# Kernel tuning notes

Measured on AMD Instinct MI355X. Metric: run time of the kernel, lower is better.

The kernel has to match this reference:

```python
import jax, jax.numpy as jnp
import numpy as np


def setup_inputs() -> dict:
    key = jax.random.key(0)
    k1, k2, k3 = jax.random.split(key, 3)
    B, N, D = 16, 2048, 128
    q = jax.random.normal(k1, (B, N, D), dtype=jnp.float32)
    k = jax.random.normal(k2, (B, D, N), dtype=jnp.float32)
    v = jax.random.normal(k3, (B, N, D), dtype=jnp.float32)
    return {"q": q, "k": k, "v": v}


def reference(q, k, v):
    # scores: [B, N, N] — note NO 1/sqrt(d) scaling, matching the source
    scores = jnp.einsum('bnd,bdm->bnm', q, k)
    probs = jax.nn.softmax(scores, axis=-1)
    out = jnp.einsum('bnm,bmd->bnd', probs, v)  # [B, N, D]
    return out
```

## Files before the change

### kernel.cpp

```cpp
#include <hip/hip_runtime.h>
#include <hip/hip_bf16.h>


typedef __attribute__((ext_vector_type(8))) _Float16 f16x8;
typedef __attribute__((ext_vector_type(4))) float f32x4;

constexpr int Bz = 16;
constexpr int Nn = 2048;
constexpr int Dd = 128;
constexpr int BM = 128;
constexpr int BN = 64;
constexpr int PK = 72;

__device__ __forceinline__ int swz(int r) { return (r ^ (r >> 3)) & 7; }

__device__ __forceinline__ uint packh2(float a, float b) {
    union { _Float16 h[2]; uint u; } p;
    p.h[0] = (_Float16)a; p.h[1] = (_Float16)b;
    return p.u;
}

__global__ __launch_bounds__(512, 2)
void fattn_kernel(const float* __restrict__ qg,
                  const float* __restrict__ kg,
                  const float* __restrict__ vg,
                  float* __restrict__ og)
{
    __shared__ ushort lds_k[BN * Dd];
    __shared__ ushort lds_v[Dd * BN];
    __shared__ ushort lds_p[8 * 16 * PK];
    uint* const lds_k32 = (uint*)lds_k;
    uint* const lds_v32 = (uint*)lds_v;

    const int bid  = blockIdx.x;
    const int xcd  = bid & 7;
    const int idx  = bid >> 3;
    const int b    = xcd * 2 + (idx >> 4);
    const int q0   = (idx & 15) * BM;
    const int tid  = threadIdx.x;
    const int wv   = tid >> 6;
    const int lane = tid & 63;
    const int quad = lane >> 4;
    const int l15  = lane & 15;

    f16x8 qf[4];
    {
        const float* qp = qg + (size_t)(b * Nn + q0 + wv * 16 + l15) * Dd + quad * 8;
        #pragma unroll
        for (int c = 0; c < 4; ++c) {
            float4 x0 = *(const float4*)(qp + c * 32);
            float4 x1 = *(const float4*)(qp + c * 32 + 4);
            const float xv[8] = {x0.x, x0.y, x0.z, x0.w, x1.x, x1.y, x1.z, x1.w};
            union { f16x8 v; _Float16 e[8]; } u;
            #pragma unroll
            for (int j = 0; j < 8; ++j) u.e[j] = (_Float16)xv[j];
            qf[c] = u.v;
        }
    }

    f32x4 accO[8];
    #pragma unroll
    for (int i = 0; i < 8; ++i) accO[i] = f32x4{0.f, 0.f, 0.f, 0.f};
    float m_i = -1e30f, l_i = 0.f;

    const int kgrp = tid & 7;
    const int krow = tid >> 3;
    const int vgrp = tid & 15;
    const int vrow = tid >> 4;

    const float* kbase = kg + (size_t)b * Dd * Nn;
    const float* vbase = vg + (size_t)b * Nn * Dd;

    float4 kr[4], vr[4];
    auto issue_loads = [&](int n0) {
        const int d0 = krow * 2;
        const float* s0 = kbase + (size_t)d0 * Nn + n0 + kgrp * 8;
        kr[0] = ((const float4*)s0)[0];
        kr[1] = ((const float4*)s0)[1];
        kr[2] = ((const float4*)(s0 + Nn))[0];
        kr[3] = ((const float4*)(s0 + Nn))[1];
        const int kk0 = vrow * 2;
        const float* t0 = vbase + (size_t)(n0 + kk0) * Dd + vgrp * 8;
        vr[0] = ((const float4*)t0)[0];
        vr[1] = ((const float4*)t0)[1];
        vr[2] = ((const float4*)(t0 + Dd))[0];
        vr[3] = ((const float4*)(t0 + Dd))[1];
    };
    auto write_lds = [&]() {
        const int d0 = krow * 2;
        const float* av = (const float*)&kr[0];
        const float* bv = (const float*)&kr[2];
        #pragma unroll
        for (int j = 0; j < 8; ++j) {
            const int n = kgrp * 8 + j;
            lds_k32[n * (Dd / 2) + ((d0 >> 1) ^ (swz(n) << 2))] = packh2(av[j], bv[j]);
        }
        const int kk0 = vrow * 2;
        const float* cv = (const float*)&vr[0];
        const float* dv = (const float*)&vr[2];
        #pragma unroll
        for (int j = 0; j < 8; ++j) {
            const int dd = vgrp * 8 + j;
            lds_v32[dd * (BN / 2) + ((kk0 >> 1) ^ (swz(dd) << 2))] = packh2(cv[j], dv[j]);
        }
    };

    issue_loads(0);

    for (int it = 0; it < Nn / BN; ++it) {
        write_lds();
        __syncthreads();

        issue_loads(((it + 1) & 31) * BN);

        f32x4 accS[4];
        #pragma unroll
        for (int kt = 0; kt < 4; ++kt) {
            f32x4 s = f32x4{0.f, 0.f, 0.f, 0.f};
            const int row = kt * 16 + l15;
            const int sw = swz(row) << 3;
            #pragma unroll
            for (int c = 0; c < 4; ++c) {
                f16x8 kf = *(const f16x8*)&lds_k[row * Dd + ((c * 32 + quad * 8) ^ sw)];
                s = __builtin_amdgcn_mfma_f32_16x16x32_f16(kf, qf[c], s, 0, 0, 0);
            }
            accS[kt] = s;
        }

        float mx = accS[0][0];
        #pragma unroll
        for (int kt = 0; kt < 4; ++kt)
            #pragma unroll
            for (int r = 0; r < 4; ++r)
                mx = fmaxf(mx, accS[kt][r]);
        mx = fmaxf(mx, __shfl_xor(mx, 16, 64));
        mx = fmaxf(mx, __shfl_xor(mx, 32, 64));
        const float mn = fmaxf(m_i, mx);
        const float alpha = __expf(m_i - mn);
        m_i = mn;
        float local = 0.f;
        #pragma unroll
        for (int kt = 0; kt < 4; ++kt)
            #pragma unroll
            for (int r = 0; r < 4; ++r) {
                const float p = __expf(accS[kt][r] - mn);
                accS[kt][r] = p;
                local += p;
            }
        l_i = l_i * alpha + local;
        #pragma unroll
        for (int dt = 0; dt < 8; ++dt)
            #pragma unroll
            for (int r = 0; r < 4; ++r)
                accO[dt][r] *= alpha;

        ushort* pl = lds_p + wv * 16 * PK;
        #pragma unroll
        for (int kt = 0; kt < 4; ++kt) {
            uint2 w;
            w.x = packh2(accS[kt][0], accS[kt][1]);
            w.y = packh2(accS[kt][2], accS[kt][3]);
            *(uint2*)(pl + l15 * PK + kt * 16 + quad * 4) = w;
        }
        f16x8 pf0 = *(const f16x8*)&pl[l15 * PK + quad * 8];
        f16x8 pf1 = *(const f16x8*)&pl[l15 * PK + 32 + quad * 8];

        #pragma unroll
        for (int dt = 0; dt < 8; ++dt) {
            const int row = dt * 16 + l15;
            const int sw = swz(row) << 3;
            f16x8 vf0 = *(const f16x8*)&lds_v[row * BN + ((quad * 8) ^ sw)];
            f16x8 vf1 = *(const f16x8*)&lds_v[row * BN + ((32 + quad * 8) ^ sw)];
            accO[dt] = __builtin_amdgcn_mfma_f32_16x16x32_f16(vf0, pf0, accO[dt], 0, 0, 0);
            accO[dt] = __builtin_amdgcn_mfma_f32_16x16x32_f16(vf1, pf1, accO[dt], 0, 0, 0);
        }
        __syncthreads();
    }

    float l = l_i;
    l += __shfl_xor(l, 16, 64);
    l += __shfl_xor(l, 32, 64);
    const float inv = 1.f / l;
    float* ob = og + (size_t)(b * Nn + q0 + wv * 16 + l15) * Dd;
    #pragma unroll
    for (int dt = 0; dt < 8; ++dt) {
        float4 val;
        val.x = accO[dt][0] * inv;
        val.y = accO[dt][1] * inv;
        val.z = accO[dt][2] * inv;
        val.w = accO[dt][3] * inv;
        *(float4*)(ob + dt * 16 + quad * 4) = val;
    }
}

extern "C" void kernel_launch(void* const* d_in, const int* in_sizes, int n_in,
                              void* d_out, int out_size, void* d_ws, size_t ws_size,
                              hipStream_t stream) {
    const float* q = (const float*)d_in[0];
    const float* k = (const float*)d_in[1];
    const float* v = (const float*)d_in[2];
    float* o = (float*)d_out;
    (void)d_ws; (void)ws_size; (void)in_sizes; (void)n_in; (void)out_size;
    fattn_kernel<<<dim3(Bz * (Nn / BM)), dim3(512), 0, stream>>>(q, k, v, o);
}
```

Before: 150.9 us.

## Warp-specialize producer/consumer waves with double-buffered LDS and 32x32 MFMA

Splits the 8 waves into 4 producer waves that load K/V from global memory, convert them to fp16 and write a double-buffered LDS tile, and 4 consumer waves that each handle 32 query rows using 32x32x16 MFMA. The KV tile shrinks to 32 keys per iteration, with a new swizzle for the V layout. The aim is to overlap global loads with compute and to use larger MFMA tiles. In exchange, half the waves do no math, there are twice as many iterations and barriers, and consumers hold more accumulator registers.

```diff
diff --git a/kernel.cpp b/kernel.cpp
--- a/kernel.cpp
+++ b/kernel.cpp
@@ -3,16 +3,17 @@
 
 
 typedef __attribute__((ext_vector_type(8))) _Float16 f16x8;
-typedef __attribute__((ext_vector_type(4))) float f32x4;
+typedef __attribute__((ext_vector_type(16))) float f32x16;
 
 constexpr int Bz = 16;
 constexpr int Nn = 2048;
 constexpr int Dd = 128;
 constexpr int BM = 128;
-constexpr int BN = 64;
-constexpr int PK = 72;
+constexpr int BN = 32;
+constexpr int PK = 40;
 
 __device__ __forceinline__ int swz(int r) { return (r ^ (r >> 3)) & 7; }
+__device__ __forceinline__ int sw4(int d) { return ((d >> 1) ^ (d >> 3)) & 3; }
 
 __device__ __forceinline__ uint packh2(float a, float b) {
     union { _Float16 h[2]; uint u; } p;
@@ -26,11 +27,9 @@
                   const float* __restrict__ vg,
                   float* __restrict__ og)
 {
-    __shared__ ushort lds_k[BN * Dd];
-    __shared__ ushort lds_v[Dd * BN];
-    __shared__ ushort lds_p[8 * 16 * PK];
-    uint* const lds_k32 = (uint*)lds_k;
-    uint* const lds_v32 = (uint*)lds_v;
+    __shared__ ushort lds_k[2][BN * Dd];
+    __shared__ ushort lds_v[2][Dd * BN];
+    __shared__ ushort lds_p[4][32 * PK];
 
     const int bid  = blockIdx.x;
     const int xcd  = bid & 7;
@@ -40,38 +39,19 @@
     const int tid  = threadIdx.x;
     const int wv   = tid >> 6;
     const int lane = tid & 63;
-    const int quad = lane >> 4;
-    const int l15  = lane & 15;
-
-    f16x8 qf[4];
-    {
-        const float* qp = qg + (size_t)(b * Nn + q0 + wv * 16 + l15) * Dd + quad * 8;
-        #pragma unroll
-        for (int c = 0; c < 4; ++c) {
-            float4 x0 = *(const float4*)(qp + c * 32);
-            float4 x1 = *(const float4*)(qp + c * 32 + 4);
-            const float xv[8] = {x0.x, x0.y, x0.z, x0.w, x1.x, x1.y, x1.z, x1.w};
-            union { f16x8 v; _Float16 e[8]; } u;
-            #pragma unroll
-            for (int j = 0; j < 8; ++j) u.e[j] = (_Float16)xv[j];
-            qf[c] = u.v;
-        }
-    }
-
-    f32x4 accO[8];
-    #pragma unroll
-    for (int i = 0; i < 8; ++i) accO[i] = f32x4{0.f, 0.f, 0.f, 0.f};
-    float m_i = -1e30f, l_i = 0.f;
-
-    const int kgrp = tid & 7;
-    const int krow = tid >> 3;
-    const int vgrp = tid & 15;
-    const int vrow = tid >> 4;
-
+    const int h    = lane >> 5;
+    const int l31  = lane & 31;
+    const bool producer = (wv >= 4);
+
+    const int ptid = (wv - 4) * 64 + lane;
+    const int kgrp = ptid & 3;
+    const int krow = ptid >> 2;
+    const int vgrp = ptid & 15;
+    const int vrow = ptid >> 4;
     const float* kbase = kg + (size_t)b * Dd * Nn;
     const float* vbase = vg + (size_t)b * Nn * Dd;
-
     float4 kr[4], vr[4];
+
     auto issue_loads = [&](int n0) {
         const int d0 = krow * 2;
         const float* s0 = kbase + (size_t)d0 * Nn + n0 + kgrp * 8;
@@ -86,110 +66,137 @@
         vr[2] = ((const float4*)(t0 + Dd))[0];
         vr[3] = ((const float4*)(t0 + Dd))[1];
     };
-    auto write_lds = [&]() {
-        const int d0 = krow * 2;
+    auto write_lds = [&](int buf) {
+        uint* kw = (uint*)lds_k[buf];
         const float* av = (const float*)&kr[0];
         const float* bv = (const float*)&kr[2];
         #pragma unroll
         for (int j = 0; j < 8; ++j) {
             const int n = kgrp * 8 + j;
-            lds_k32[n * (Dd / 2) + ((d0 >> 1) ^ (swz(n) << 2))] = packh2(av[j], bv[j]);
-        }
-        const int kk0 = vrow * 2;
+            kw[n * (Dd / 2) + (krow ^ (swz(n) << 2))] = packh2(av[j], bv[j]);
+        }
+        uint* vw = (uint*)lds_v[buf];
         const float* cv = (const float*)&vr[0];
         const float* dv = (const float*)&vr[2];
         #pragma unroll
         for (int j = 0; j < 8; ++j) {
             const int dd = vgrp * 8 + j;
-            lds_v32[dd * (BN / 2) + ((kk0 >> 1) ^ (swz(dd) << 2))] = packh2(cv[j], dv[j]);
+            vw[dd * (BN / 2) + (vrow ^ (sw4(dd) << 2))] = packh2(cv[j], dv[j]);
         }
     };
 
-    issue_loads(0);
-
-    for (int it = 0; it < Nn / BN; ++it) {
-        write_lds();
+    f16x8 qf[8];
+    if (!producer) {
+        const float* qp = qg + (size_t)(b * Nn + q0 + wv * 32 + l31) * Dd + h * 8;
+        #pragma unroll
+        for (int c = 0; c < 8; ++c) {
+            float4 x0 = *(const float4*)(qp + c * 16);
+            float4 x1 = *(const float4*)(qp + c * 16 + 4);
+            const float xv[8] = {x0.x, x0.y, x0.z, x0.w, x1.x, x1.y, x1.z, x1.w};
+            union { f16x8 v; _Float16 e[8]; } u;
+            #pragma unroll
+            for (int j = 0; j < 8; ++j) u.e[j] = (_Float16)xv[j];
+            qf[c] = u.v;
+        }
+    }
+    f32x16 accO[4];
+    #pragma unroll
+    for (int dt = 0; dt < 4; ++dt)
+        #pragma unroll
+        for (int r = 0; r < 16; ++r) accO[dt][r] = 0.f;
+    float m_i = -1e30f, l_i = 0.f;
+
+    if (producer) {
+        issue_loads(0);
+        write_lds(0);
+    }
+    __syncthreads();
+
+    constexpr int ITERS = Nn / BN;
+    for (int it = 0; it < ITERS; ++it) {
+        const int cur = it & 1;
+        if (producer) {
+            if (it + 1 < ITERS) {
+                issue_loads((it + 1) * BN);
+                write_lds(cur ^ 1);
+            }
+        } else {
+            const ushort* kb = lds_k[cur];
+            const ushort* vb = lds_v[cur];
+
+            f32x16 accS;
+            #pragma unroll
+            for (int r = 0; r < 16; ++r) accS[r] = 0.f;
+            {
+                const int kkrow = l31;
+                const int sw = swz(kkrow) << 3;
+                #pragma unroll
+                for (int c = 0; c < 8; ++c) {
+                    f16x8 kf = *(const f16x8*)&kb[kkrow * Dd + ((c * 16 + h * 8) ^ sw)];
+                    accS = __builtin_amdgcn_mfma_f32_32x32x16_f16(kf, qf[c], accS, 0, 0, 0);
+                }
+            }
+
+            float mx = accS[0];
+            #pragma unroll
+            for (int r = 1; r < 16; ++r) mx = fmaxf(mx, accS[r]);
+            mx = fmaxf(mx, __shfl_xor(mx, 32, 64));
+            const float mn = fmaxf(m_i, mx);
+            const float alpha = __expf(m_i - mn);
+            m_i = mn;
+            float local = 0.f;
+            #pragma unroll
+            for (int r = 0; r < 16; ++r) {
+                const float p = __expf(accS[r] - mn);
+                accS[r] = p;
+                local += p;
+            }
+            l_i = l_i * alpha + local;
+            #pragma unroll
+            for (int dt = 0; dt < 4; ++dt)
+                #pragma unroll
+                for (int r = 0; r < 16; ++r) accO[dt][r] *= alpha;
+
+            ushort* pl = lds_p[wv];
+            #pragma unroll
+            for (int g = 0; g < 4; ++g) {
+                uint2 w;
+                w.x = packh2(accS[4 * g + 0], accS[4 * g + 1]);
+                w.y = packh2(accS[4 * g + 2], accS[4 * g + 3]);
+                *(uint2*)(pl + l31 * PK + 8 * g + 4 * h) = w;
+            }
+            f16x8 pf0 = *(const f16x8*)&pl[l31 * PK + 8 * h];
+            f16x8 pf1 = *(const f16x8*)&pl[l31 * PK + 16 + 8 * h];
+
+            #pragma unroll
+            for (int dt = 0; dt < 4; ++dt) {
+                const int drow = dt * 32 + l31;
+                const int sv = sw4(drow) << 3;
+                f16x8 vf0 = *(const f16x8*)&vb[drow * BN + ((8 * h) ^ sv)];
+                f16x8 vf1 = *(const f16x8*)&vb[drow * BN + ((16 + 8 * h) ^ sv)];
+                accO[dt] = __builtin_amdgcn_mfma_f32_32x32x16_f16(vf0, pf0, accO[dt], 0, 0, 0);
+                accO[dt] = __builtin_amdgcn_mfma_f32_32x32x16_f16(vf1, pf1, accO[dt], 0, 0, 0);
+            }
+        }
         __syncthreads();
-
-        issue_loads(((it + 1) & 31) * BN);
-
-        f32x4 accS[4];
-        #pragma unroll
-        for (int kt = 0; kt < 4; ++kt) {
-            f32x4 s = f32x4{0.f, 0.f, 0.f, 0.f};
-            const int row = kt * 16 + l15;
-            const int sw = swz(row) << 3;
-            #pragma unroll
-            for (int c = 0; c < 4; ++c) {
-                f16x8 kf = *(const f16x8*)&lds_k[row * Dd + ((c * 32 + quad * 8) ^ sw)];
-                s = __builtin_amdgcn_mfma_f32_16x16x32_f16(kf, qf[c], s, 0, 0, 0);
-            }
-            accS[kt] = s;
-        }
-
-        float mx = accS[0][0];
-        #pragma unroll
-        for (int kt = 0; kt < 4; ++kt)
-            #pragma unroll
-            for (int r = 0; r < 4; ++r)
-                mx = fmaxf(mx, accS[kt][r]);
-        mx = fmaxf(mx, __shfl_xor(mx, 16, 64));
-        mx = fmaxf(mx, __shfl_xor(mx, 32, 64));
-        const float mn = fmaxf(m_i, mx);
-        const float alpha = __expf(m_i - mn);
-        m_i = mn;
-        float local = 0.f;
-        #pragma unroll
-        for (int kt = 0; kt < 4; ++kt)
-            #pragma unroll
-            for (int r = 0; r < 4; ++r) {
-                const float p = __expf(accS[kt][r] - mn);
-                accS[kt][r] = p;
-                local += p;
-            }
-        l_i = l_i * alpha + local;
-        #pragma unroll
-        for (int dt = 0; dt < 8; ++dt)
-            #pragma unroll
-            for (int r = 0; r < 4; ++r)
-                accO[dt][r] *= alpha;
-
-        ushort* pl = lds_p + wv * 16 * PK;
-        #pragma unroll
-        for (int kt = 0; kt < 4; ++kt) {
-            uint2 w;
-            w.x = packh2(accS[kt][0], accS[kt][1]);
-            w.y = packh2(accS[kt][2], accS[kt][3]);
-            *(uint2*)(pl + l15 * PK + kt * 16 + quad * 4) = w;
-        }
-        f16x8 pf0 = *(const f16x8*)&pl[l15 * PK + quad * 8];
-        f16x8 pf1 = *(const f16x8*)&pl[l15 * PK + 32 + quad * 8];
-
-        #pragma unroll
-        for (int dt = 0; dt < 8; ++dt) {
-            const int row = dt * 16 + l15;
-            const int sw = swz(row) << 3;
-            f16x8 vf0 = *(const f16x8*)&lds_v[row * BN + ((quad * 8) ^ sw)];
-            f16x8 vf1 = *(const f16x8*)&lds_v[row * BN + ((32 + quad * 8) ^ sw)];
-            accO[dt] = __builtin_amdgcn_mfma_f32_16x16x32_f16(vf0, pf0, accO[dt], 0, 0, 0);
-            accO[dt] = __builtin_amdgcn_mfma_f32_16x16x32_f16(vf1, pf1, accO[dt], 0, 0, 0);
-        }
-        __syncthreads();
-    }
-
-    float l = l_i;
-    l += __shfl_xor(l, 16, 64);
-    l += __shfl_xor(l, 32, 64);
-    const float inv = 1.f / l;
-    float* ob = og + (size_t)(b * Nn + q0 + wv * 16 + l15) * Dd;
-    #pragma unroll
-    for (int dt = 0; dt < 8; ++dt) {
-        float4 val;
-        val.x = accO[dt][0] * inv;
-        val.y = accO[dt][1] * inv;
-        val.z = accO[dt][2] * inv;
-        val.w = accO[dt][3] * inv;
-        *(float4*)(ob + dt * 16 + quad * 4) = val;
+    }
+
+    if (!producer) {
+        float l = l_i + __shfl_xor(l_i, 32, 64);
+        const float inv = 1.f / l;
+        float* ob = og + (size_t)(b * Nn + q0 + wv * 32 + l31) * Dd;
+        #pragma unroll
+        for (int dt = 0; dt < 4; ++dt) {
+            #pragma unroll
+            for (int g = 0; g < 4; ++g) {
+                float4 val;
+                val.x = accO[dt][4 * g + 0] * inv;
+                val.y = accO[dt][4 * g + 1] * inv;
+                val.z = accO[dt][4 * g + 2] * inv;
+                val.w = accO[dt][4 * g + 3] * inv;
+                *(float4*)(ob + dt * 32 + 8 * g + 4 * h) = val;
+            }
+        }
     }
 }
 
```

Result: faster. 145.0 us (-3.9%).

## Split KV range across two wave groups per block with LDS merge

Applied to the files above, without the earlier changes.

Halves the query tile to 64 rows and KV tile to 32, and splits each block's 8 waves into two groups that each process half of the key/value sequence, merging the partial softmax states through shared memory at the end. This doubles the grid size and raises the occupancy hint to 4 blocks per CU, aiming for more parallelism and latency hiding. The register prefetch of the next tile is dropped, so global loads are no longer overlapped with compute. Each block also reuses every K/V tile across fewer query rows, which adds global traffic and an extra merge step.

```diff
diff --git a/kernel.cpp b/kernel.cpp
--- a/kernel.cpp
+++ b/kernel.cpp
@@ -8,11 +8,14 @@
 constexpr int Bz = 16;
 constexpr int Nn = 2048;
 constexpr int Dd = 128;
-constexpr int BM = 128;
-constexpr int BN = 64;
-constexpr int PK = 72;
+constexpr int BM = 64;
+constexpr int BN = 32;
+constexpr int HALF = Nn / 2;
+constexpr int ITERS = HALF / BN;
+constexpr int PK = 40;
 
 __device__ __forceinline__ int swz(int r) { return (r ^ (r >> 3)) & 7; }
+__device__ __forceinline__ int sw4(int d) { return ((d >> 1) ^ (d >> 3)) & 3; }
 
 __device__ __forceinline__ uint packh2(float a, float b) {
     union { _Float16 h[2]; uint u; } p;
@@ -20,32 +23,44 @@
     return p.u;
 }
 
-__global__ __launch_bounds__(512, 2)
+__global__ __launch_bounds__(512, 4)
 void fattn_kernel(const float* __restrict__ qg,
                   const float* __restrict__ kg,
                   const float* __restrict__ vg,
                   float* __restrict__ og)
 {
-    __shared__ ushort lds_k[BN * Dd];
-    __shared__ ushort lds_v[Dd * BN];
-    __shared__ ushort lds_p[8 * 16 * PK];
-    uint* const lds_k32 = (uint*)lds_k;
-    uint* const lds_v32 = (uint*)lds_v;
+    __shared__ ushort smem[21504];
 
     const int bid  = blockIdx.x;
     const int xcd  = bid & 7;
     const int idx  = bid >> 3;
-    const int b    = xcd * 2 + (idx >> 4);
-    const int q0   = (idx & 15) * BM;
+    const int b    = xcd * 2 + (idx >> 5);
+    const int q0   = (idx & 31) * BM;
     const int tid  = threadIdx.x;
     const int wv   = tid >> 6;
     const int lane = tid & 63;
     const int quad = lane >> 4;
     const int l15  = lane & 15;
+    const int w    = wv & 3;
+    const int g    = wv >> 2;
+
+    ushort* const kb = smem + g * 4096;
+    ushort* const vb = smem + 8192 + g * 4096;
+    ushort* const pl = smem + 16384 + wv * 640;
+    uint* const kw = (uint*)kb;
+    uint* const vw = (uint*)vb;
+
+    const int gtid = tid & 255;
+    const int kgN = (gtid & 3) * 8;
+    const int kdp = gtid >> 2;
+    const int vgD = (gtid & 15) * 8;
+    const int vkp = gtid >> 4;
+    const float* kbase = kg + (size_t)b * Dd * Nn;
+    const float* vbase = vg + (size_t)b * Nn * Dd;
 
     f16x8 qf[4];
     {
-        const float* qp = qg + (size_t)(b * Nn + q0 + wv * 16 + l15) * Dd + quad * 8;
+        const float* qp = qg + (size_t)(b * Nn + q0 + w * 16 + l15) * Dd + quad * 8;
         #pragma unroll
         for (int c = 0; c < 4; ++c) {
             float4 x0 = *(const float4*)(qp + c * 32);
@@ -57,82 +72,53 @@
             qf[c] = u.v;
         }
     }
-
     f32x4 accO[8];
     #pragma unroll
     for (int i = 0; i < 8; ++i) accO[i] = f32x4{0.f, 0.f, 0.f, 0.f};
     float m_i = -1e30f, l_i = 0.f;
 
-    const int kgrp = tid & 7;
-    const int krow = tid >> 3;
-    const int vgrp = tid & 15;
-    const int vrow = tid >> 4;
-
-    const float* kbase = kg + (size_t)b * Dd * Nn;
-    const float* vbase = vg + (size_t)b * Nn * Dd;
-
-    float4 kr[4], vr[4];
-    auto issue_loads = [&](int n0) {
-        const int d0 = krow * 2;
-        const float* s0 = kbase + (size_t)d0 * Nn + n0 + kgrp * 8;
-        kr[0] = ((const float4*)s0)[0];
-        kr[1] = ((const float4*)s0)[1];
-        kr[2] = ((const float4*)(s0 + Nn))[0];
-        kr[3] = ((const float4*)(s0 + Nn))[1];
-        const int kk0 = vrow * 2;
-        const float* t0 = vbase + (size_t)(n0 + kk0) * Dd + vgrp * 8;
-        vr[0] = ((const float4*)t0)[0];
-        vr[1] = ((const float4*)t0)[1];
-        vr[2] = ((const float4*)(t0 + Dd))[0];
-        vr[3] = ((const float4*)(t0 + Dd))[1];
-    };
-    auto write_lds = [&]() {
-        const int d0 = krow * 2;
-        const float* av = (const float*)&kr[0];
-        const float* bv = (const float*)&kr[2];
-        #pragma unroll
-        for (int j = 0; j < 8; ++j) {
-            const int n = kgrp * 8 + j;
-            lds_k32[n * (Dd / 2) + ((d0 >> 1) ^ (swz(n) << 2))] = packh2(av[j], bv[j]);
-        }
-        const int kk0 = vrow * 2;
-        const float* cv = (const float*)&vr[0];
-        const float* dv = (const float*)&vr[2];
-        #pragma unroll
-        for (int j = 0; j < 8; ++j) {
-            const int dd = vgrp * 8 + j;
-            lds_v32[dd * (BN / 2) + ((kk0 >> 1) ^ (swz(dd) << 2))] = packh2(cv[j], dv[j]);
-        }
-    };
-
-    issue_loads(0);
-
-    for (int it = 0; it < Nn / BN; ++it) {
-        write_lds();
+    for (int it = 0; it < ITERS; ++it) {
+        const int n0 = g * HALF + it * BN;
+        {
+            const float* s0 = kbase + (size_t)(2 * kdp) * Nn + n0 + kgN;
+            float4 a0 = ((const float4*)s0)[0], a1 = ((const float4*)s0)[1];
+            float4 b0 = ((const float4*)(s0 + Nn))[0], b1 = ((const float4*)(s0 + Nn))[1];
+            const float av[8] = {a0.x, a0.y, a0.z, a0.w, a1.x, a1.y, a1.z, a1.w};
+            const float bv[8] = {b0.x, b0.y, b0.z, b0.w, b1.x, b1.y, b1.z, b1.w};
+            #pragma unroll
+            for (int j = 0; j < 8; ++j) {
+                const int n = kgN + j;
+                kw[n * 64 + (kdp ^ (swz(n) << 2))] = packh2(av[j], bv[j]);
+            }
+            const float* t0 = vbase + (size_t)(n0 + 2 * vkp) * Dd + vgD;
+            float4 c0 = ((const float4*)t0)[0], c1 = ((const float4*)t0)[1];
+            float4 d0 = ((const float4*)(t0 + Dd))[0], d1 = ((const float4*)(t0 + Dd))[1];
+            const float cv[8] = {c0.x, c0.y, c0.z, c0.w, c1.x, c1.y, c1.z, c1.w};
+            const float dv[8] = {d0.x, d0.y, d0.z, d0.w, d1.x, d1.y, d1.z, d1.w};
+            #pragma unroll
+            for (int j = 0; j < 8; ++j) {
+                const int dd = vgD + j;
+                vw[dd * 16 + (vkp ^ (sw4(dd) << 2))] = packh2(cv[j], dv[j]);
+            }
+        }
         __syncthreads();
 
-        issue_loads(((it + 1) & 31) * BN);
-
-        f32x4 accS[4];
-        #pragma unroll
-        for (int kt = 0; kt < 4; ++kt) {
+        f32x4 accS[2];
+        #pragma unroll
+        for (int kt = 0; kt < 2; ++kt) {
             f32x4 s = f32x4{0.f, 0.f, 0.f, 0.f};
             const int row = kt * 16 + l15;
             const int sw = swz(row) << 3;
             #pragma unroll
             for (int c = 0; c < 4; ++c) {
-                f16x8 kf = *(const f16x8*)&lds_k[row * Dd + ((c * 32 + quad * 8) ^ sw)];
+                f16x8 kf = *(const f16x8*)&kb[row * 128 + ((c * 32 + quad * 8) ^ sw)];
                 s = __builtin_amdgcn_mfma_f32_16x16x32_f16(kf, qf[c], s, 0, 0, 0);
             }
             accS[kt] = s;
         }
 
-        float mx = accS[0][0];
-        #pragma unroll
-        for (int kt = 0; kt < 4; ++kt)
-            #pragma unroll
-            for (int r = 0; r < 4; ++r)
-                mx = fmaxf(mx, accS[kt][r]);
+        float mx = fmaxf(fmaxf(fmaxf(accS[0][0], accS[0][1]), fmaxf(accS[0][2], accS[0][3])),
+                         fmaxf(fmaxf(accS[1][0], accS[1][1]), fmaxf(accS[1][2], accS[1][3])));
         mx = fmaxf(mx, __shfl_xor(mx, 16, 64));
         mx = fmaxf(mx, __shfl_xor(mx, 32, 64));
         const float mn = fmaxf(m_i, mx);
@@ -140,7 +126,7 @@
         m_i = mn;
         float local = 0.f;
         #pragma unroll
-        for (int kt = 0; kt < 4; ++kt)
+        for (int kt = 0; kt < 2; ++kt)
             #pragma unroll
             for (int r = 0; r < 4; ++r) {
                 const float p = __expf(accS[kt][r] - mn);
@@ -151,45 +137,67 @@
         #pragma unroll
         for (int dt = 0; dt < 8; ++dt)
             #pragma unroll
-            for (int r = 0; r < 4; ++r)
-                accO[dt][r] *= alpha;
-
-        ushort* pl = lds_p + wv * 16 * PK;
-        #pragma unroll
-        for (int kt = 0; kt < 4; ++kt) {
-            uint2 w;
-            w.x = packh2(accS[kt][0], accS[kt][1]);
-            w.y = packh2(accS[kt][2], accS[kt][3]);
-            *(uint2*)(pl + l15 * PK + kt * 16 + quad * 4) = w;
-        }
-        f16x8 pf0 = *(const f16x8*)&pl[l15 * PK + quad * 8];
-        f16x8 pf1 = *(const f16x8*)&pl[l15 * PK + 32 + quad * 8];
+            for (int r = 0; r < 4; ++r) accO[dt][r] *= alpha;
+
+        #pragma unroll
+        for (int kt = 0; kt < 2; ++kt) {
+            uint2 pw;
+            pw.x = packh2(accS[kt][0], accS[kt][1]);
+            pw.y = packh2(accS[kt][2], accS[kt][3]);
+            *(uint2*)(pl + l15 * PK + kt * 16 + quad * 4) = pw;
+        }
+        f16x8 pf = *(const f16x8*)&pl[l15 * PK + quad * 8];
 
         #pragma unroll
         for (int dt = 0; dt < 8; ++dt) {
-            const int row = dt * 16 + l15;
-            const int sw = swz(row) << 3;
-            f16x8 vf0 = *(const f16x8*)&lds_v[row * BN + ((quad * 8) ^ sw)];
-            f16x8 vf1 = *(const f16x8*)&lds_v[row * BN + ((32 + quad * 8) ^ sw)];
-            accO[dt] = __builtin_amdgcn_mfma_f32_16x16x32_f16(vf0, pf0, accO[dt], 0, 0, 0);
-            accO[dt] = __builtin_amdgcn_mfma_f32_16x16x32_f16(vf1, pf1, accO[dt], 0, 0, 0);
+            const int drow = dt * 16 + l15;
+            const int sv = sw4(drow) << 3;
+            f16x8 vf = *(const f16x8*)&vb[drow * 32 + ((quad * 8) ^ sv)];
+            accO[dt] = __builtin_amdgcn_mfma_f32_16x16x32_f16(vf, pf, accO[dt], 0, 0, 0);
         }
         __syncthreads();
     }
 
-    float l = l_i;
-    l += __shfl_xor(l, 16, 64);
-    l += __shfl_xor(l, 32, 64);
-    const float inv = 1.f / l;
-    float* ob = og + (size_t)(b * Nn + q0 + wv * 16 + l15) * Dd;
-    #pragma unroll
-    for (int dt = 0; dt < 8; ++dt) {
-        float4 val;
-        val.x = accO[dt][0] * inv;
-        val.y = accO[dt][1] * inv;
-        val.z = accO[dt][2] * inv;
-        val.w = accO[dt][3] * inv;
-        *(float4*)(ob + dt * 16 + quad * 4) = val;
+    float lr = l_i;
+    lr += __shfl_xor(lr, 16, 64);
+    lr += __shfl_xor(lr, 32, 64);
+
+    float* mergef = (float*)smem;
+    float* mlf = (float*)(smem + 16384);
+    if (g == 1) {
+        #pragma unroll
+        for (int dt = 0; dt < 8; ++dt) {
+            const int gr = (dt * 4 + quad) ^ ((l15 & 7) << 2);
+            float4 val;
+            val.x = accO[dt][0]; val.y = accO[dt][1];
+            val.z = accO[dt][2]; val.w = accO[dt][3];
+            *(float4*)(mergef + w * 2048 + l15 * 128 + gr * 4) = val;
+        }
+        if (quad == 0) {
+            mlf[w * 32 + l15 * 2]     = m_i;
+            mlf[w * 32 + l15 * 2 + 1] = lr;
+        }
+    }
+    __syncthreads();
+    if (g == 0) {
+        const float mB = mlf[w * 32 + l15 * 2];
+        const float lB = mlf[w * 32 + l15 * 2 + 1];
+        const float m  = fmaxf(m_i, mB);
+        const float eA = __expf(m_i - m);
+        const float eB = __expf(mB - m);
+        const float inv = 1.f / (lr * eA + lB * eB);
+        float* ob = og + (size_t)(b * Nn + q0 + w * 16 + l15) * Dd;
+        #pragma unroll
+        for (int dt = 0; dt < 8; ++dt) {
+            const int gr = (dt * 4 + quad) ^ ((l15 & 7) << 2);
+            float4 vB = *(const float4*)(mergef + w * 2048 + l15 * 128 + gr * 4);
+            float4 val;
+            val.x = (accO[dt][0] * eA + vB.x * eB) * inv;
+            val.y = (accO[dt][1] * eA + vB.y * eB) * inv;
+            val.z = (accO[dt][2] * eA + vB.z * eB) * inv;
+            val.w = (accO[dt][3] * eA + vB.w * eB) * inv;
+            *(float4*)(ob + dt * 16 + quad * 4) = val;
+        }
     }
 }
 
```

Result: slower. 172.3 us (+14.1%).
